# Optimization experiments

Hardware: AMD Instinct MI355X
Metric: run time of the kernel (lower is better)

Reference implementation:

```python
import jax, jax.numpy as jnp
import numpy as np

B, TX, DH, U2 = 32, 2048, 512, 1024  # batch, src len, decoder dim, 2*units

def setup_inputs() -> dict:
    key = jax.random.key(0)
    ks = jax.random.split(key, 8)
    a = jax.random.normal(ks[0], (B, TX, U2), jnp.float32)
    h = jax.random.normal(ks[1], (B, DH), jnp.float32)
    coverage = jax.random.uniform(ks[2], (B, TX), jnp.float32)
    X_mask = jax.random.randint(ks[3], (B, TX, 1), 0, 2).astype(bool)
    s = 1.0 / np.sqrt(U2)
    Wa = jax.random.normal(ks[4], (U2, U2), jnp.float32) * s
    Wh_w = jax.random.normal(ks[5], (DH, U2), jnp.float32) / np.sqrt(DH)
    Wh_b = jnp.zeros((U2,), jnp.float32)
    Wc = jax.random.normal(ks[6], (1, U2), jnp.float32)
    v = jax.random.normal(ks[7], (U2, 1), jnp.float32) * s
    return {"a": a, "h": h, "coverage": coverage, "X_mask": X_mask,
            "Wa": Wa, "Wh_w": Wh_w, "Wh_b": Wh_b, "Wc": Wc, "v": v,
            "use_coverage": 1, "use_masking": 1}

def reference(a, h, coverage, X_mask, Wa, Wh_w, Wh_b, Wc, v,
              use_coverage, use_masking):
    # encoder features: [B,Tx,2u]
    enc = jnp.einsum('btd,de->bte', a, Wa)
    # decoder features broadcast over Tx (RepeatVector): [B,1,2u]
    dec = (h @ Wh_w + Wh_b)[:, None, :]
    feats = enc + dec
    if use_coverage:
        # coverage [B,Tx] -> [B,Tx,1] @ Wc[1,2u] == outer broadcast
        feats = feats + coverage[:, :, None] * Wc[0]
    e = jnp.tanh(feats) @ v                      # [B,Tx,1]
    alpha = jax.nn.softmax(e, axis=1)            # softmax over Tx
    if use_masking:
        alpha = jnp.where(X_mask, alpha, 0.0)
        alpha_sum = jnp.sum(alpha, axis=1)       # [B,1]
        alpha = jnp.squeeze(alpha, -1) / alpha_sum  # [B,Tx]
        alpha = alpha[:, :, None]
    context = jnp.sum(alpha * a, axis=1)[:, None, :]  # [B,1,2u]
    return context, jnp.squeeze(alpha, -1)
```

## Files before the change

kernel.cpp:

```cpp
#include <hip/hip_runtime.h>
#include <hip/hip_bf16.h>

#define BB  32
#define TXX 2048
#define DHH 512
#define UU  1024
#define MM  (BB*TXX)

typedef __attribute__((ext_vector_type(8))) short s8v;
typedef __attribute__((ext_vector_type(4))) float f4v;

#define GLDS16(g, l)                                                        \
  __builtin_amdgcn_global_load_lds(                                         \
      (const __attribute__((address_space(1))) void*)(g),                   \
      (__attribute__((address_space(3))) void*)(l), 16, 0, 0)

__device__ __forceinline__ ushort f2bf(float f) {
  return __builtin_bit_cast(ushort, __float2bfloat16(f));
}
__device__ __forceinline__ float bf2f(ushort u) {
  unsigned x = ((unsigned)u) << 16;
  return __builtin_bit_cast(float, x);
}

__device__ __forceinline__ float tanh_fast(float x) {
  float ax = fabsf(x);
  float e2 = __expf(-2.0f * ax);
  float t = (1.0f - e2) * __builtin_amdgcn_rcpf(1.0f + e2);
  return copysignf(t, x);
}

__device__ __forceinline__ int ldsu(int frag, int kh, int i15) {
  return (frag << 6) | (kh << 4) | (i15 ^ (kh << 2));
}

#define PREP_A2BF   32768
#define PREP_WT     256
#define PREP_DEC    128
#define PREP_GRID   (PREP_A2BF + PREP_WT + PREP_DEC)

__global__ __launch_bounds__(256) void prep_kernel(
    const float* __restrict__ a, ushort* __restrict__ abf,
    const float* __restrict__ Wa, ushort* __restrict__ WaT,
    const float* __restrict__ h, const float* __restrict__ Whw,
    const float* __restrict__ Whb, float* __restrict__ dec) {
  __shared__ float Ts[64][65];
  const int bid = blockIdx.x;
  const int tid = threadIdx.x;

  if (bid < PREP_A2BF) {
    const size_t i = ((size_t)bid * 256 + tid) * 8;
    float4 v0 = *(const float4*)(a + i);
    float4 v1 = *(const float4*)(a + i + 4);
    ushort u[8] = {f2bf(v0.x), f2bf(v0.y), f2bf(v0.z), f2bf(v0.w),
                   f2bf(v1.x), f2bf(v1.y), f2bf(v1.z), f2bf(v1.w)};
    *(uint4*)(abf + i) = *(const uint4*)u;
  } else if (bid < PREP_A2BF + PREP_WT) {
    const int wb = bid - PREP_A2BF;
    const int jb = wb & 15, kb = wb >> 4;
    const int c = tid & 63, r0 = tid >> 6;
#pragma unroll
    for (int i = 0; i < 16; ++i) {
      int kl = r0 + 4 * i;
      Ts[c][kl] = Wa[(size_t)(kb * 64 + kl) * UU + jb * 64 + c];
    }
    __syncthreads();
#pragma unroll
    for (int i = 0; i < 16; ++i) {
      int jl = r0 + 4 * i;
      WaT[(size_t)(jb * 64 + jl) * UU + kb * 64 + c] = f2bf(Ts[jl][c]);
    }
  } else {
    const int db = bid - PREP_A2BF - PREP_WT;
    const int b = db >> 2, c = db & 3;
    float* hs = &Ts[0][0];
    for (int k = tid; k < DHH; k += 256) hs[k] = h[b * DHH + k];
    __syncthreads();
    const int j = c * 256 + tid;
    float acc = Whb[j];
#pragma unroll 8
    for (int k = 0; k < DHH; ++k) acc = fmaf(hs[k], Whw[(size_t)k * UU + j], acc);
    dec[b * UU + j] = acc;
  }
}

__global__ __launch_bounds__(256) void watrans_kernel(
    const float* __restrict__ Wa, ushort* __restrict__ WaT) {
  __shared__ float Ts[64][65];
  const int jb = blockIdx.x & 15, kb = blockIdx.x >> 4;
  const int c = threadIdx.x & 63, r0 = threadIdx.x >> 6;
#pragma unroll
  for (int i = 0; i < 16; ++i) {
    int kl = r0 + 4 * i;
    Ts[c][kl] = Wa[(size_t)(kb * 64 + kl) * UU + jb * 64 + c];
  }
  __syncthreads();
#pragma unroll
  for (int i = 0; i < 16; ++i) {
    int jl = r0 + 4 * i;
    WaT[(size_t)(jb * 64 + jl) * UU + kb * 64 + c] = f2bf(Ts[jl][c]);
  }
}

__global__ __launch_bounds__(256) void dec_kernel(
    const float* __restrict__ h, const float* __restrict__ Whw,
    const float* __restrict__ Whb, float* __restrict__ dec) {
  const int b = blockIdx.x >> 2, c = blockIdx.x & 3;
  __shared__ float hs[DHH];
  for (int k = threadIdx.x; k < DHH; k += 256) hs[k] = h[b * DHH + k];
  __syncthreads();
  const int j = c * 256 + threadIdx.x;
  float acc = Whb[j];
#pragma unroll 8
  for (int k = 0; k < DHH; ++k) acc = fmaf(hs[k], Whw[(size_t)k * UU + j], acc);
  dec[b * UU + j] = acc;
}

__global__ __launch_bounds__(512, 1) void e_mfma8_kernel(
    const ushort* __restrict__ abf, const ushort* __restrict__ WaT,
    const float* __restrict__ dec, const float* __restrict__ cov,
    const float* __restrict__ Wc, const float* __restrict__ v,
    const int* __restrict__ use_cov_p, float* __restrict__ partial) {
  __shared__ __align__(16) ushort aS[32768];
  __shared__ __align__(16) ushort bS[32768];
  __shared__ float dec_s[256], v_s[256], wc_s[256], cov_s[256];
  __shared__ float peL[4][256];

  const int tid = threadIdx.x;
  const int lane = tid & 63;
  const int w = tid >> 6;
  const int wm = w >> 2, wn = w & 3;

  const int x = blockIdx.x & 7;
  const int r = blockIdx.x >> 3;
  const int nt = r & 3;
  const int mt = (r >> 2) * 8 + x;

  const int j0 = nt * 256;
  const int row0 = mt * 256;
  const int b = row0 >> 11;
  const int trow0 = row0 & (TXX - 1);

  if (tid < 256) {
    dec_s[tid] = dec[b * UU + j0 + tid];
    v_s[tid] = v[j0 + tid];
    wc_s[tid] = Wc[j0 + tid];
    cov_s[tid] = (*use_cov_p) ? cov[b * TXX + trow0 + tid] : 0.0f;
  }

  f4v acc[8][4];
#pragma unroll
  for (int mi = 0; mi < 8; ++mi)
#pragma unroll
    for (int ni = 0; ni < 4; ++ni) acc[mi][ni] = (f4v){0.f, 0.f, 0.f, 0.f};

  const ushort* __restrict__ aT = abf + (size_t)row0 * UU;
  const ushort* __restrict__ bT = WaT + (size_t)j0 * UU;
  const int i15 = lane & 15, khl = lane >> 4;

  auto stageA = [&](int kt, int ns, int kf) {
#pragma unroll
    for (int l = 0; l < 2; ++l) {
      const int frag = l * 8 + w;
      GLDS16(aT + (size_t)(frag * 16 + i15) * UU + kt * 64 + kf * 32 + khl * 8,
             &aS[ns * 16384 + kf * 8192 + (l * 512 + w * 64) * 8]);
    }
  };
  auto stageB = [&](int kt, int ns, int kf) {
#pragma unroll
    for (int l = 0; l < 2; ++l) {
      const int frag = l * 8 + w;
      GLDS16(bT + (size_t)(frag * 16 + i15) * UU + kt * 64 + kf * 32 + khl * 8,
             &bS[ns * 16384 + kf * 8192 + (l * 512 + w * 64) * 8]);
    }
  };
  auto readA = [&](s8v af[4], int slot, int kf, int mh) {
#pragma unroll
    for (int q = 0; q < 4; ++q) {
      const int frag = wm * 8 + mh * 4 + q;
      af[q] = *(const s8v*)&aS[slot * 16384 + kf * 8192 + frag * 512 + lane * 8];
    }
  };
  auto readB = [&](s8v bf[4], int slot, int kf) {
#pragma unroll
    for (int q = 0; q < 4; ++q) {
      const int frag = wn * 4 + q;
      bf[q] = *(const s8v*)&bS[slot * 16384 + kf * 8192 + frag * 512 + lane * 8];
    }
  };

#define MFMA16(MH)                                                          \
  do {                                                                      \
    __builtin_amdgcn_s_setprio(1);                                          \
    _Pragma("unroll")                                                       \
    for (int q = 0; q < 4; ++q)                                             \
      _Pragma("unroll")                                                     \
      for (int ni = 0; ni < 4; ++ni)                                        \
        acc[(MH)*4 + q][ni] = __builtin_amdgcn_mfma_f32_16x16x32_bf16(      \
            af[q], bf[ni], acc[(MH)*4 + q][ni], 0, 0, 0);                   \
    __builtin_amdgcn_s_setprio(0);                                          \
  } while (0)

#define VMBAR(N)                                                            \
  asm volatile("s_waitcnt vmcnt(" #N ")" ::: "memory");                     \
  __builtin_amdgcn_s_barrier();                                             \
  __builtin_amdgcn_sched_barrier(0)

  stageA(0, 0, 0); stageB(0, 0, 0); stageA(0, 0, 1); stageB(0, 0, 1);

  for (int t = 0; t < 16; ++t) {
    const int slot = t & 1, ns = slot ^ 1;
    s8v af[4], bf[4];
    if (t < 15) { stageA(t + 1, ns, 0); VMBAR(6); } else { VMBAR(4); }
    readB(bf, slot, 0);
    readA(af, slot, 0, 0);
    MFMA16(0);
    if (t < 15) stageB(t + 1, ns, 0);
    readA(af, slot, 0, 1);
    MFMA16(1);
    if (t < 15) { stageA(t + 1, ns, 1); VMBAR(6); } else { VMBAR(0); }
    readB(bf, slot, 1);
    readA(af, slot, 1, 0);
    MFMA16(0);
    if (t < 15) stageB(t + 1, ns, 1);
    readA(af, slot, 1, 1);
    MFMA16(1);
  }
#undef VMBAR
#undef MFMA16

  const int lj = lane & 15, lk = lane >> 4;
#pragma unroll
  for (int mi = 0; mi < 8; ++mi) {
#pragma unroll
    for (int r2 = 0; r2 < 4; ++r2) {
      const int rowl = wm * 128 + mi * 16 + lk * 4 + r2;
      const float cv = cov_s[rowl];
      float s = 0.f;
#pragma unroll
      for (int ni = 0; ni < 4; ++ni) {
        const int jl = wn * 64 + ni * 16 + lj;
        float f = acc[mi][ni][r2] + dec_s[jl] + cv * wc_s[jl];
        s += v_s[jl] * tanh_fast(f);
      }
      s += __shfl_xor(s, 1); s += __shfl_xor(s, 2);
      s += __shfl_xor(s, 4); s += __shfl_xor(s, 8);
      if (lj == 0) peL[wn][rowl] = s;
    }
  }
  __syncthreads();
  if (tid < 256)
    partial[(size_t)nt * MM + row0 + tid] =
        peL[0][tid] + peL[1][tid] + peL[2][tid] + peL[3][tid];
}

__device__ __forceinline__ void e_epilogue8(
    f4v acc[4][4], const float* dec_s, const float* v_s, const float* wc_s,
    const float* cov_s, float peL[2][128], int lane, int wm, int wn,
    float* __restrict__ partial, int nt, int row0, int tid) {
  const int lj = lane & 15, lk = lane >> 4;
#pragma unroll
  for (int mi = 0; mi < 4; ++mi) {
#pragma unroll
    for (int r = 0; r < 4; ++r) {
      const int rowl = (wm << 6) + (mi << 4) + (lk << 2) + r;
      const float cv = cov_s[rowl];
      float s = 0.f;
#pragma unroll
      for (int ni = 0; ni < 4; ++ni) {
        const int jl = (wn << 6) + (ni << 4) + lj;
        float f = acc[mi][ni][r] + dec_s[jl] + cv * wc_s[jl];
        s += v_s[jl] * tanh_fast(f);
      }
      s += __shfl_xor(s, 1); s += __shfl_xor(s, 2);
      s += __shfl_xor(s, 4); s += __shfl_xor(s, 8);
      if (lj == 0) peL[wn][rowl] = s;
    }
  }
  __syncthreads();
  if (tid < 128)
    partial[(size_t)nt * MM + row0 + tid] = peL[0][tid] + peL[1][tid];
}

__global__ __launch_bounds__(256) void e_mfma_slow_kernel(
    const float* __restrict__ a, const ushort* __restrict__ WaT,
    const float* __restrict__ dec, const float* __restrict__ cov,
    const float* __restrict__ Wc, const float* __restrict__ v,
    const int* __restrict__ use_cov_p, float* __restrict__ partial) {
  __shared__ __align__(16) ushort aS[4096];
  __shared__ __align__(16) ushort bS[4096];
  __shared__ float dec_s[128], v_s[128], wc_s[128], cov_s[128];
  __shared__ float peL[2][128];

  const int tid = threadIdx.x;
  const int lane = tid & 63;
  const int wid = tid >> 6;
  const int wm = wid >> 1, wn = wid & 1;

  const int x = blockIdx.x & 7;
  const int q = blockIdx.x >> 3;
  const int nt = q & 7;
  const int mt = (q >> 3) * 8 + x;

  const int j0 = nt * 128;
  const int row0 = mt * 128;
  const int b = row0 >> 11;
  const int trow0 = row0 & (TXX - 1);

  if (tid < 128) {
    dec_s[tid] = dec[b * UU + j0 + tid];
    v_s[tid] = v[j0 + tid];
    wc_s[tid] = Wc[j0 + tid];
    cov_s[tid] = (*use_cov_p) ? cov[b * TXX + trow0 + tid] : 0.0f;
  }

  f4v zero = {0.f, 0.f, 0.f, 0.f};
  f4v acc[4][4];
#pragma unroll
  for (int mi = 0; mi < 4; ++mi)
#pragma unroll
    for (int ni = 0; ni < 4; ++ni) acc[mi][ni] = zero;

  const float* __restrict__ aRow = a + (size_t)row0 * UU;
  const int arow = tid >> 3;
  const int kq = (tid & 7) * 4;
  const int jrow = tid >> 2;
  const int kc = tid & 3;

  for (int ks = 0; ks < 32; ++ks) {
    const int k0 = ks * 32;
#pragma unroll
    for (int l = 0; l < 4; ++l) {
      const int row = l * 32 + arow;
      float4 va = *(const float4*)(aRow + (size_t)row * UU + k0 + kq);
      ushort4 ub = make_ushort4(f2bf(va.x), f2bf(va.y), f2bf(va.z), f2bf(va.w));
      const int unit = ldsu(row >> 4, kq >> 3, row & 15);
      *(ushort4*)&aS[unit * 8 + (kq & 7)] = ub;
    }
#pragma unroll
    for (int l = 0; l < 2; ++l) {
      const int jr = l * 64 + jrow;
      uint4 wv = *(const uint4*)(WaT + (size_t)(j0 + jr) * UU + k0 + kc * 8);
      *(uint4*)&bS[ldsu(jr >> 4, kc, jr & 15) * 8] = wv;
    }
    __syncthreads();
    s8v af[4], bff[4];
    const int kh = lane >> 4, i15 = lane & 15;
#pragma unroll
    for (int mi = 0; mi < 4; ++mi)
      af[mi] = *(const s8v*)&aS[ldsu((wm << 2) + mi, kh, i15) * 8];
#pragma unroll
    for (int ni = 0; ni < 4; ++ni)
      bff[ni] = *(const s8v*)&bS[ldsu((wn << 2) + ni, kh, i15) * 8];
#pragma unroll
    for (int mi = 0; mi < 4; ++mi)
#pragma unroll
      for (int ni = 0; ni < 4; ++ni)
        acc[mi][ni] = __builtin_amdgcn_mfma_f32_16x16x32_bf16(af[mi], bff[ni], acc[mi][ni], 0, 0, 0);
    __syncthreads();
  }

  e_epilogue8(acc, dec_s, v_s, wc_s, cov_s, peL, lane, wm, wn, partial, nt, row0, tid);
}

__global__ __launch_bounds__(256) void softmax_kernel(
    const float* __restrict__ partial, const void* __restrict__ mask,
    const int* __restrict__ use_mask_p, float* __restrict__ alpha, int npart) {
  int b = blockIdx.x;
  int tid = threadIdx.x;
  int lane = tid & 63, wv = tid >> 6;
  const unsigned char* m8 = (const unsigned char*)mask;
  const int* m32 = (const int*)mask;
  int um = *use_mask_p;

  __shared__ int isBoolS;
  if (tid == 0) isBoolS = 0;

  __shared__ float es[TXX];
  for (int t = tid; t < TXX; t += 256) {
    float s = 0.f;
    for (int nt = 0; nt < npart; ++nt) s += partial[(size_t)nt * MM + b * TXX + t];
    es[t] = s;
  }
  __syncthreads();
  {
    uint4 qq = ((const uint4*)mask)[tid];
    unsigned nz = (qq.x | qq.y | qq.z | qq.w) & 0xFFFFFF00u;
    if (nz) atomicOr(&isBoolS, 1);
  }
  __syncthreads();
  const int isBool = isBoolS;

  float m = -1e30f;
  for (int t = tid; t < TXX; t += 256) m = fmaxf(m, es[t]);
#pragma unroll
  for (int o = 32; o > 0; o >>= 1) m = fmaxf(m, __shfl_xor(m, o, 64));
  __shared__ float redm[4];
  if (lane == 0) redm[wv] = m;
  __syncthreads();
  m = fmaxf(fmaxf(redm[0], redm[1]), fmaxf(redm[2], redm[3]));

  float s = 0.f;
  for (int t = tid; t < TXX; t += 256) {
    float w = __expf(es[t] - m);
    if (um) {
      int mv = isBool ? (int)m8[b * TXX + t] : m32[b * TXX + t];
      if (mv == 0) w = 0.f;
    }
    s += w;
  }
#pragma unroll
  for (int o = 32; o > 0; o >>= 1) s += __shfl_xor(s, o, 64);
  __shared__ float reds[4];
  if (lane == 0) reds[wv] = s;
  __syncthreads();
  s = reds[0] + reds[1] + reds[2] + reds[3];
  float inv = 1.0f / s;

  for (int t = tid; t < TXX; t += 256) {
    float w = __expf(es[t] - m);
    if (um) {
      int mv = isBool ? (int)m8[b * TXX + t] : m32[b * TXX + t];
      if (mv == 0) w = 0.f;
    }
    alpha[b * TXX + t] = w * inv;
  }
}

__global__ __launch_bounds__(256) void context_bf_kernel(
    const ushort* __restrict__ abf, const float* __restrict__ alpha,
    float* __restrict__ cpart) {
  const int b = blockIdx.x >> 4;
  const int ts = blockIdx.x & 15;
  const int th = threadIdx.x >> 7;
  const int c = threadIdx.x & 127;
  const int dc = c * 8;
  const ushort* __restrict__ ab = abf + (size_t)(b * TXX + ts * 128) * UU + dc;
  const float* __restrict__ alb = alpha + b * TXX + ts * 128;
  float acc[8] = {0.f, 0.f, 0.f, 0.f, 0.f, 0.f, 0.f, 0.f};
  for (int t = th; t < 128; t += 2) {
    float al = alb[t];
    union { uint4 q; ushort us[8]; } Q;
    Q.q = *(const uint4*)(ab + (size_t)t * UU);
#pragma unroll
    for (int u = 0; u < 8; ++u) acc[u] = fmaf(al, bf2f(Q.us[u]), acc[u]);
  }
  __shared__ float s2[2][128][8];
#pragma unroll
  for (int u = 0; u < 8; ++u) s2[th][c][u] = acc[u];
  __syncthreads();
  if (th == 0) {
    float o[8];
#pragma unroll
    for (int u = 0; u < 8; ++u) o[u] = s2[0][c][u] + s2[1][c][u];
    float* dst = cpart + (size_t)(ts * BB + b) * UU + dc;
    *(float4*)dst = make_float4(o[0], o[1], o[2], o[3]);
    *(float4*)(dst + 4) = make_float4(o[4], o[5], o[6], o[7]);
  }
}

__global__ __launch_bounds__(256) void context_f32_kernel(
    const float* __restrict__ a, const float* __restrict__ alpha,
    float* __restrict__ cpart) {
  const int b = blockIdx.x >> 4;
  const int ts = blockIdx.x & 15;
  const int d4 = threadIdx.x * 4;
  const float* __restrict__ ab  = a + (size_t)(b * TXX + ts * 128) * UU;
  const float* __restrict__ alb = alpha + b * TXX + ts * 128;
  float4 acc = {0.f, 0.f, 0.f, 0.f};
  for (int t = 0; t < 128; t += 4) {
#pragma unroll
    for (int u = 0; u < 4; ++u) {
      float al = alb[t + u];
      float4 va = *(const float4*)(ab + (size_t)(t + u) * UU + d4);
      acc.x = fmaf(al, va.x, acc.x);
      acc.y = fmaf(al, va.y, acc.y);
      acc.z = fmaf(al, va.z, acc.z);
      acc.w = fmaf(al, va.w, acc.w);
    }
  }
  *(float4*)(cpart + (size_t)(ts * BB + b) * UU + d4) = acc;
}

__global__ __launch_bounds__(256) void ctx_reduce_kernel(
    const float* __restrict__ cpart, float* __restrict__ ctx) {
  int i = blockIdx.x * 256 + threadIdx.x;
  float s = 0.f;
#pragma unroll
  for (int ts = 0; ts < 16; ++ts) s += cpart[(size_t)ts * BB * UU + i];
  ctx[i] = s;
}

extern "C" void kernel_launch(void* const* d_in, const int* in_sizes, int n_in,
                              void* d_out, int out_size, void* d_ws, size_t ws_size,
                              hipStream_t stream) {
  const float* a   = (const float*)d_in[0];
  const float* h   = (const float*)d_in[1];
  const float* cov = (const float*)d_in[2];
  const void*  msk = d_in[3];
  const float* Wa  = (const float*)d_in[4];
  const float* Whw = (const float*)d_in[5];
  const float* Whb = (const float*)d_in[6];
  const float* Wc  = (const float*)d_in[7];
  const float* v   = (const float*)d_in[8];
  const int* use_cov  = (const int*)d_in[9];
  const int* use_mask = (const int*)d_in[10];

  float*  dec     = (float*)d_ws;
  ushort* WaT     = (ushort*)((char*)d_ws + 131072);
  float*  partial = (float*)((char*)d_ws + 131072 + 2097152);
  float*  cpart   = partial;
  ushort* abf     = (ushort*)((char*)d_ws + 4325376);
  const size_t need = 4325376 + (size_t)MM * UU * 2;

  float* ctx   = (float*)d_out;
  float* alpha = (float*)d_out + BB * UU;

  if (ws_size >= need) {
    prep_kernel<<<PREP_GRID, 256, 0, stream>>>(a, abf, Wa, WaT, h, Whw, Whb, dec);
    e_mfma8_kernel<<<(MM / 256) * 4, 512, 0, stream>>>(abf, WaT, dec, cov, Wc, v, use_cov, partial);
    softmax_kernel<<<BB, 256, 0, stream>>>(partial, msk, use_mask, alpha, 4);
    context_bf_kernel<<<BB * 16, 256, 0, stream>>>(abf, alpha, cpart);
  } else {
    watrans_kernel<<<256, 256, 0, stream>>>(Wa, WaT);
    dec_kernel<<<BB * 4, 256, 0, stream>>>(h, Whw, Whb, dec);
    e_mfma_slow_kernel<<<(MM / 128) * 8, 256, 0, stream>>>(a, WaT, dec, cov, Wc, v, use_cov, partial);
    softmax_kernel<<<BB, 256, 0, stream>>>(partial, msk, use_mask, alpha, 8);
    context_f32_kernel<<<BB * 16, 256, 0, stream>>>(a, alpha, cpart);
  }
  ctx_reduce_kernel<<<BB * UU / 256, 256, 0, stream>>>(cpart, ctx);
}
```

Baseline: 309.4 us.

## Deepen GEMM prefetch pipeline to stage half-tiles further ahead

Restructures the main K-loop of the fused attention-score GEMM so global-to-LDS loads run further ahead. The second half of tile t+1 is staged right after the first barrier, and the first half of tile t+2 is staged into the just-consumed slot half, with waitcnt thresholds adjusted to match. This gives each load more time to land before it is consumed, hiding memory latency behind MFMA work. The cost is more outstanding loads and a more intricate slot-reuse ordering, which could race if the barrier placement is wrong.

Measured after the change: 360.6 us. 1.17x slower.

```diff
diff --git a/kernel.cpp b/kernel.cpp
--- a/kernel.cpp
+++ b/kernel.cpp
@@ -206,26 +206,34 @@
   __builtin_amdgcn_s_barrier();                                             \
   __builtin_amdgcn_sched_barrier(0)
 
-  stageA(0, 0, 0); stageB(0, 0, 0); stageA(0, 0, 1); stageB(0, 0, 1);
-
-  for (int t = 0; t < 16; ++t) {
-    const int slot = t & 1, ns = slot ^ 1;
-    s8v af[4], bf[4];
-    if (t < 15) { stageA(t + 1, ns, 0); VMBAR(6); } else { VMBAR(4); }
-    readB(bf, slot, 0);
-    readA(af, slot, 0, 0);
-    MFMA16(0);
-    if (t < 15) stageB(t + 1, ns, 0);
-    readA(af, slot, 0, 1);
-    MFMA16(1);
-    if (t < 15) { stageA(t + 1, ns, 1); VMBAR(6); } else { VMBAR(0); }
-    readB(bf, slot, 1);
-    readA(af, slot, 1, 0);
-    MFMA16(0);
-    if (t < 15) stageB(t + 1, ns, 1);
-    readA(af, slot, 1, 1);
-    MFMA16(1);
-  }
+#define TILE(T, G0, G1, S1, S2)                                             \
+  do {                                                                      \
+    const int slot = (T) & 1, nsl = slot ^ 1;                               \
+    s8v af[4], bf[4];                                                       \
+    VMBAR(G0);                                                              \
+    if (S1) { stageA((T) + 1, nsl, 1); stageB((T) + 1, nsl, 1); }           \
+    readB(bf, slot, 0);                                                     \
+    readA(af, slot, 0, 0);                                                  \
+    MFMA16(0);                                                              \
+    readA(af, slot, 0, 1);                                                  \
+    MFMA16(1);                                                              \
+    VMBAR(G1);                                                              \
+    if (S2) { stageA((T) + 2, slot, 0); stageB((T) + 2, slot, 0); }         \
+    readB(bf, slot, 1);                                                     \
+    readA(af, slot, 1, 0);                                                  \
+    MFMA16(0);                                                              \
+    readA(af, slot, 1, 1);                                                  \
+    MFMA16(1);                                                              \
+  } while (0)
+
+  stageA(0, 0, 0); stageB(0, 0, 0);
+  stageA(0, 0, 1); stageB(0, 0, 1);
+  stageA(1, 1, 0); stageB(1, 1, 0);
+
+  for (int t = 0; t < 14; ++t) TILE(t, 8, 8, 1, 1);
+  TILE(14, 8, 8, 1, 0);
+  TILE(15, 4, 0, 0, 0);
+#undef TILE
 #undef VMBAR
 #undef MFMA16
 
```

## Halve the K-tile to shrink LDS and raise launch-bound occupancy

Applied to the files above, without the earlier changes.

The K step of the bf16 MFMA GEMM drops from 64 to 32, halving the LDS staging buffers for A and B, and the loop now runs 32 iterations instead of 16. Launch bounds change from (512,1) to (512,4) to allow more resident blocks per CU. The aim is better latency hiding through occupancy. In exchange there are twice as many barriers and waits per unit of work, and register pressure may force spills, since 128 accumulator floats per thread must fit under the tighter bound.

Measured after the change: 1.063 ms. 3.44x slower.

```diff
diff --git a/kernel.cpp b/kernel.cpp
--- a/kernel.cpp
+++ b/kernel.cpp
@@ -116,13 +116,13 @@
   dec[b * UU + j] = acc;
 }
 
-__global__ __launch_bounds__(512, 1) void e_mfma8_kernel(
+__global__ __launch_bounds__(512, 4) void e_mfma8_kernel(
     const ushort* __restrict__ abf, const ushort* __restrict__ WaT,
     const float* __restrict__ dec, const float* __restrict__ cov,
     const float* __restrict__ Wc, const float* __restrict__ v,
     const int* __restrict__ use_cov_p, float* __restrict__ partial) {
-  __shared__ __align__(16) ushort aS[32768];
-  __shared__ __align__(16) ushort bS[32768];
+  __shared__ __align__(16) ushort aS[16384];
+  __shared__ __align__(16) ushort bS[16384];
   __shared__ float dec_s[256], v_s[256], wc_s[256], cov_s[256];
   __shared__ float peL[4][256];
 
@@ -158,34 +158,34 @@
   const ushort* __restrict__ bT = WaT + (size_t)j0 * UU;
   const int i15 = lane & 15, khl = lane >> 4;
 
-  auto stageA = [&](int kt, int ns, int kf) {
+  auto stageA = [&](int kt, int ns) {
 #pragma unroll
     for (int l = 0; l < 2; ++l) {
       const int frag = l * 8 + w;
-      GLDS16(aT + (size_t)(frag * 16 + i15) * UU + kt * 64 + kf * 32 + khl * 8,
-             &aS[ns * 16384 + kf * 8192 + (l * 512 + w * 64) * 8]);
+      GLDS16(aT + (size_t)(frag * 16 + i15) * UU + kt * 32 + khl * 8,
+             &aS[ns * 8192 + (l * 512 + w * 64) * 8]);
     }
   };
-  auto stageB = [&](int kt, int ns, int kf) {
+  auto stageB = [&](int kt, int ns) {
 #pragma unroll
     for (int l = 0; l < 2; ++l) {
       const int frag = l * 8 + w;
-      GLDS16(bT + (size_t)(frag * 16 + i15) * UU + kt * 64 + kf * 32 + khl * 8,
-             &bS[ns * 16384 + kf * 8192 + (l * 512 + w * 64) * 8]);
+      GLDS16(bT + (size_t)(frag * 16 + i15) * UU + kt * 32 + khl * 8,
+             &bS[ns * 8192 + (l * 512 + w * 64) * 8]);
     }
   };
-  auto readA = [&](s8v af[4], int slot, int kf, int mh) {
+  auto readA = [&](s8v af[4], int slot, int mh) {
 #pragma unroll
     for (int q = 0; q < 4; ++q) {
       const int frag = wm * 8 + mh * 4 + q;
-      af[q] = *(const s8v*)&aS[slot * 16384 + kf * 8192 + frag * 512 + lane * 8];
+      af[q] = *(const s8v*)&aS[slot * 8192 + frag * 512 + lane * 8];
     }
   };
-  auto readB = [&](s8v bf[4], int slot, int kf) {
+  auto readB = [&](s8v bf[4], int slot) {
 #pragma unroll
     for (int q = 0; q < 4; ++q) {
       const int frag = wn * 4 + q;
-      bf[q] = *(const s8v*)&bS[slot * 16384 + kf * 8192 + frag * 512 + lane * 8];
+      bf[q] = *(const s8v*)&bS[slot * 8192 + frag * 512 + lane * 8];
     }
   };
 
@@ -206,24 +206,17 @@
   __builtin_amdgcn_s_barrier();                                             \
   __builtin_amdgcn_sched_barrier(0)
 
-  stageA(0, 0, 0); stageB(0, 0, 0); stageA(0, 0, 1); stageB(0, 0, 1);
-
-  for (int t = 0; t < 16; ++t) {
+  stageA(0, 0); stageB(0, 0);
+
+  for (int t = 0; t < 32; ++t) {
     const int slot = t & 1, ns = slot ^ 1;
     s8v af[4], bf[4];
-    if (t < 15) { stageA(t + 1, ns, 0); VMBAR(6); } else { VMBAR(4); }
-    readB(bf, slot, 0);
-    readA(af, slot, 0, 0);
+    if (t < 31) { stageA(t + 1, ns); VMBAR(2); } else { VMBAR(0); }
+    readB(bf, slot);
+    readA(af, slot, 0);
     MFMA16(0);
-    if (t < 15) stageB(t + 1, ns, 0);
-    readA(af, slot, 0, 1);
-    MFMA16(1);
-    if (t < 15) { stageA(t + 1, ns, 1); VMBAR(6); } else { VMBAR(0); }
-    readB(bf, slot, 1);
-    readA(af, slot, 1, 0);
-    MFMA16(0);
-    if (t < 15) stageB(t + 1, ns, 1);
-    readA(af, slot, 1, 1);
+    if (t < 31) stageB(t + 1, ns);
+    readA(af, slot, 1);
     MFMA16(1);
   }
 #undef VMBAR
```
